# Performance work log

Measured on AMD Instinct MI355X. Metric: run time of the kernel, lower is better.

The kernel has to match this reference:

```python
import jax, jax.numpy as jnp
import numpy as np

N, TI, ENC_DIM, DEC_DIM, ATT_DIM = 32, 2000, 512, 512, 512


def setup_inputs() -> dict:
    key = jax.random.key(0)
    ks = jax.random.split(key, 8)
    enc_pad = jax.random.normal(ks[0], (N, TI, ENC_DIM), dtype=jnp.float32)
    dec_prev = jax.random.normal(ks[1], (N, DEC_DIM), dtype=jnp.float32)
    ali_prev = jax.random.uniform(ks[2], (N, TI), dtype=jnp.float32)
    # lengths in [Ti//2, Ti], force one full-length row (module uses max(enc_len) as mask width)
    enc_len = jax.random.randint(ks[3], (N,), TI // 2, TI + 1)
    enc_len = enc_len.at[0].set(TI)
    # learned params (nn.Linear layout: W [out, in])
    s_e = 1.0 / np.sqrt(ENC_DIM)
    s_d = 1.0 / np.sqrt(DEC_DIM)
    s_a = 1.0 / np.sqrt(ATT_DIM)
    W_enc = jax.random.uniform(ks[4], (ATT_DIM, ENC_DIM), minval=-s_e, maxval=s_e, dtype=jnp.float32)
    b_enc = jax.random.uniform(ks[5], (ATT_DIM,), minval=-s_e, maxval=s_e, dtype=jnp.float32)
    W_dec = jax.random.uniform(ks[6], (ATT_DIM, DEC_DIM), minval=-s_d, maxval=s_d, dtype=jnp.float32)
    w_v = jax.random.uniform(ks[7], (ATT_DIM,), minval=-s_a, maxval=s_a, dtype=jnp.float32)
    return {"enc_pad": enc_pad, "enc_len": enc_len, "dec_prev": dec_prev,
            "ali_prev": ali_prev, "W_enc": W_enc, "b_enc": b_enc,
            "W_dec": W_dec, "w_v": w_v}


def reference(enc_pad, enc_len, dec_prev, ali_prev, W_enc, b_enc, W_dec, w_v):
    # enc_part: N x Ti x A  (enc_proj with bias)
    enc_part = jnp.einsum('ntd,ad->nta', enc_pad, W_enc) + b_enc
    # dec_part: N x A  (dec_proj, no bias)
    dec_part = jnp.einsum('nd,ad->na', dec_prev, W_dec)
    # additive score e = w^T tanh(enc_part + dec_part): N x Ti
    e = jnp.einsum('nta,a->nt', jnp.tanh(enc_part + dec_part[:, None, :]), w_v)
    # padding mask: positions >= enc_len are masked
    mask = jnp.arange(e.shape[1]) >= enc_len[:, None]  # N x Ti
    e = jnp.where(mask, -jnp.inf, e)
    ali = jax.nn.softmax(e, axis=1)  # N x Ti
    ctx = jnp.einsum('nt,ntd->nd', ali, enc_pad)  # N x D_enc
    return (ali, ctx)
```

## Files before the change

### kernel.cpp

```cpp
#include <hip/hip_runtime.h>
#include <stdint.h>


#define NB  32
#define TI  2000
#define ED  512
#define AD  512
#define M_TOT (NB * TI)
#define NSPLIT 20
#define TCHUNK (TI / NSPLIT)
#define MTS 500
#define NKS 16

using f16x8 = __attribute__((ext_vector_type(8))) _Float16;
using f32x4 = __attribute__((ext_vector_type(4))) float;

#define GLD16(g, l)                                                     \
    __builtin_amdgcn_global_load_lds(                                   \
        (const __attribute__((address_space(1))) void*)(g),             \
        (__attribute__((address_space(3))) void*)(l), 16, 0, 0)

__device__ __forceinline__ float fast_tanh(float s) {
    s = fminf(fmaxf(s, -15.f), 15.f);
    float t = __expf(2.f * s);
    return __fdividef(t - 1.f, t + 1.f);
}

__device__ __forceinline__ f16x8 cvt8(float4 a, float4 b) {
    f16x8 h;
    h[0] = (_Float16)a.x; h[1] = (_Float16)a.y; h[2] = (_Float16)a.z; h[3] = (_Float16)a.w;
    h[4] = (_Float16)b.x; h[5] = (_Float16)b.y; h[6] = (_Float16)b.z; h[7] = (_Float16)b.w;
    return h;
}

__global__ void k_wconvert(const float* __restrict__ Wenc, _Float16* __restrict__ W16,
                           const float* __restrict__ dec_prev, const float* __restrict__ W_dec,
                           const float* __restrict__ b_enc, float* __restrict__ db) {
    __shared__ float xd[ED];
    int bx = blockIdx.x;
    int tid = threadIdx.x;
    if (bx >= 128) {
        int n = bx - 128;
        for (int k = tid; k < ED; k += 256) xd[k] = dec_prev[n * ED + k];
        __syncthreads();
        for (int a = tid; a < AD; a += 256) {
            const float* wr = W_dec + (size_t)a * ED;
            float s = 0.f;
#pragma unroll 8
            for (int k = 0; k < ED; k += 4) {
                float4 w = *(const float4*)(wr + k);
                s += xd[k] * w.x + xd[k + 1] * w.y + xd[k + 2] * w.z + xd[k + 3] * w.w;
            }
            db[n * AD + a] = s + b_enc[a];
        }
        return;
    }
    int idx  = bx * 4096 + tid * 16;
    int slab = idx >> 14;
    int o    = idx & 16383;
    int r    = o >> 6;
    int q    = o & 63;
    int a    = (slab >> 4) * 256 + r;
    int k    = (slab & 15) * 32 + (q >> 1);
    const float* s = Wenc + (size_t)a * ED + k;
    float4 x0 = *(const float4*)s;
    float4 x1 = *(const float4*)(s + 4);
    *(f16x8*)((char*)W16 + idx) = cvt8(x0, x1);
}

__global__ void k_decdb(const float* __restrict__ dec_prev,
                        const float* __restrict__ W_dec,
                        const float* __restrict__ b_enc,
                        float* __restrict__ db) {
    int n = blockIdx.x;
    __shared__ float xd[ED];
    for (int k = threadIdx.x; k < ED; k += 256) xd[k] = dec_prev[n * ED + k];
    __syncthreads();
    for (int a = threadIdx.x; a < AD; a += 256) {
        const float* wr = W_dec + (size_t)a * ED;
        float s = 0.f;
#pragma unroll 8
        for (int k = 0; k < ED; k += 4) {
            float4 w = *(const float4*)(wr + k);
            s += xd[k] * w.x + xd[k + 1] * w.y + xd[k + 2] * w.z + xd[k + 3] * w.w;
        }
        db[n * AD + a] = s + b_enc[a];
    }
}

__launch_bounds__(256, 2)
__global__ void k_score256(const float* __restrict__ enc, const _Float16* __restrict__ W16,
                           const float* __restrict__ db, const float* __restrict__ wv,
                           float* __restrict__ e_part) {
    __shared__ alignas(16) char As[16384];
    __shared__ alignas(16) char Bs[16384];

    int fid = blockIdx.x;
    int g = fid >> 4, r = fid & 15;
    int at2 = r >> 3;
    int mt  = g * 8 + (r & 7);
    if (mt >= MTS) return;

    const int tid  = threadIdx.x;
    const int lane = tid & 63;
    const int wn   = (tid >> 6) & 3;
    const int m0   = mt * 128;
    const int a0   = at2 * 256;
    const int lr   = lane & 15;
    const int gk   = lane >> 4;

    const char* wbase = (const char*)W16 + ((size_t)(at2 * 16) << 14);

    const int sr0 = tid >> 3;
    const int sq  = (tid & 7) * 16;

    f32x4 acc[8][4];
#pragma unroll
    for (int rb = 0; rb < 8; ++rb)
#pragma unroll
        for (int cb = 0; cb < 4; ++cb) acc[rb][cb] = (f32x4){0.f, 0.f, 0.f, 0.f};

    for (int ks = 0; ks < NKS; ++ks) {
#pragma unroll
        for (int i = 0; i < 4; ++i) {
            int rr = i * 32 + sr0;
            const float* gsrc = enc + (size_t)(m0 + rr) * ED + ks * 32
                                + ((sq ^ ((rr & 7) << 4)) >> 2);
            GLD16(gsrc, As + i * 4096 + tid * 16);
        }
        {
            const char* wsl = wbase + (ks << 14);
#pragma unroll
            for (int j = 0; j < 4; ++j)
                GLD16(wsl + j * 4096 + tid * 16, Bs + j * 4096 + tid * 16);
        }
        __syncthreads();

        {
            f16x8 aF[8], bF[4];
#pragma unroll
            for (int rb = 0; rb < 8; ++rb) {
                int row  = rb * 16 + lr;
                int base = row * 128 + gk * 32;
                int sw   = (row & 7) << 4;
                f32x4 lo = *(const f32x4*)(As + (base ^ sw));
                f32x4 hi = *(const f32x4*)(As + ((base + 16) ^ sw));
                f16x8 h;
                h[0] = (_Float16)lo[0]; h[1] = (_Float16)lo[1];
                h[2] = (_Float16)lo[2]; h[3] = (_Float16)lo[3];
                h[4] = (_Float16)hi[0]; h[5] = (_Float16)hi[1];
                h[6] = (_Float16)hi[2]; h[7] = (_Float16)hi[3];
                aF[rb] = h;
            }
#pragma unroll
            for (int cb = 0; cb < 4; ++cb) {
                int brow = wn * 64 + cb * 16 + lr;
                bF[cb] = *(const f16x8*)(Bs + brow * 64 + gk * 16);
            }
            __builtin_amdgcn_s_setprio(1);
#pragma unroll
            for (int rb = 0; rb < 8; ++rb)
#pragma unroll
                for (int cb = 0; cb < 4; ++cb)
                    acc[rb][cb] = __builtin_amdgcn_mfma_f32_16x16x32_f16(
                        aF[rb], bF[cb], acc[rb][cb], 0, 0, 0);
            __builtin_amdgcn_s_setprio(0);
        }
        __syncthreads();
    }

    float* e_red = (float*)As;
    float wvv[4];
#pragma unroll
    for (int cb = 0; cb < 4; ++cb) wvv[cb] = wv[a0 + wn * 64 + cb * 16 + lr];

#pragma unroll
    for (int rb = 0; rb < 8; ++rb) {
#pragma unroll
        for (int i = 0; i < 4; ++i) {
            int row_local = rb * 16 + gk * 4 + i;
            int m = m0 + row_local;
            int n = m / TI;
            const float* dbp = db + (size_t)n * AD + a0 + wn * 64;
            float rs = 0.f;
#pragma unroll
            for (int cb = 0; cb < 4; ++cb) {
                float s = acc[rb][cb][i] + dbp[cb * 16 + lr];
                rs += fast_tanh(s) * wvv[cb];
            }
            rs += __shfl_xor(rs, 1);
            rs += __shfl_xor(rs, 2);
            rs += __shfl_xor(rs, 4);
            rs += __shfl_xor(rs, 8);
            if (lr == 0) e_red[wn * 128 + row_local] = rs;
        }
    }
    __syncthreads();
    if (tid < 128)
        e_part[(size_t)at2 * M_TOT + m0 + tid] =
            e_red[tid] + e_red[128 + tid] + e_red[256 + tid] + e_red[384 + tid];
}

__launch_bounds__(256, 2)
__global__ void k_score_fb(const float* __restrict__ X, const float* __restrict__ W,
                           const float* __restrict__ db, const float* __restrict__ wv,
                           float* __restrict__ e_part) {
    __shared__ alignas(16) _Float16 Xs[128][72];
    __shared__ alignas(16) _Float16 Ws[128][72];
    __shared__ float e_red[2][128];

    const int tid = threadIdx.x, lane = tid & 63, wid = tid >> 6;
    const int wr = wid >> 1, wc = wid & 1;
    const int m0 = blockIdx.x * 128, a0 = blockIdx.y * 128;

    f32x4 acc[4][4];
#pragma unroll
    for (int rb = 0; rb < 4; ++rb)
#pragma unroll
        for (int cb = 0; cb < 4; ++cb) acc[rb][cb] = (f32x4){0.f, 0.f, 0.f, 0.f};

    const int lr = lane & 15;
    const int lk = (lane >> 4) << 3;

    for (int kt = 0; kt < ED; kt += 64) {
#pragma unroll
        for (int i = 0; i < 4; ++i) {
            int idx = tid + i * 256, r = idx >> 3, c = (idx & 7) << 3;
            const float* gx = X + (size_t)(m0 + r) * ED + kt + c;
            float4 x0 = *(const float4*)gx, x1 = *(const float4*)(gx + 4);
            *(f16x8*)&Xs[r][c] = cvt8(x0, x1);
            const float* gw = W + (size_t)(a0 + r) * ED + kt + c;
            float4 w0 = *(const float4*)gw, w1 = *(const float4*)(gw + 4);
            *(f16x8*)&Ws[r][c] = cvt8(w0, w1);
        }
        __syncthreads();
#pragma unroll
        for (int kb = 0; kb < 64; kb += 32) {
            f16x8 aF[4], bF[4];
#pragma unroll
            for (int rb = 0; rb < 4; ++rb) aF[rb] = *(const f16x8*)&Xs[wr * 64 + rb * 16 + lr][kb + lk];
#pragma unroll
            for (int cb = 0; cb < 4; ++cb) bF[cb] = *(const f16x8*)&Ws[wc * 64 + cb * 16 + lr][kb + lk];
#pragma unroll
            for (int rb = 0; rb < 4; ++rb)
#pragma unroll
                for (int cb = 0; cb < 4; ++cb)
                    acc[rb][cb] = __builtin_amdgcn_mfma_f32_16x16x32_f16(aF[rb], bF[cb], acc[rb][cb], 0, 0, 0);
        }
        __syncthreads();
    }

    const int lg = lane >> 4;
    float wvv[4];
#pragma unroll
    for (int cb = 0; cb < 4; ++cb) wvv[cb] = wv[a0 + wc * 64 + cb * 16 + lr];
#pragma unroll
    for (int rb = 0; rb < 4; ++rb) {
#pragma unroll
        for (int i = 0; i < 4; ++i) {
            int row_local = wr * 64 + rb * 16 + lg * 4 + i;
            int m = m0 + row_local;
            int n = m / TI;
            const float* dbp = db + (size_t)n * AD + a0 + wc * 64;
            float rs = 0.f;
#pragma unroll
            for (int cb = 0; cb < 4; ++cb) {
                float s = acc[rb][cb][i] + dbp[cb * 16 + lr];
                rs += fast_tanh(s) * wvv[cb];
            }
            rs += __shfl_xor(rs, 1);
            rs += __shfl_xor(rs, 2);
            rs += __shfl_xor(rs, 4);
            rs += __shfl_xor(rs, 8);
            if (lr == 0) e_red[wc][row_local] = rs;
        }
    }
    __syncthreads();
    if (tid < 128)
        e_part[(size_t)blockIdx.y * M_TOT + m0 + tid] = e_red[0][tid] + e_red[1][tid];
}

__global__ void k_softmax(const float* __restrict__ e_part,
                          const int* __restrict__ enc_len,
                          float* __restrict__ ali, int nparts) {
    int n = blockIdx.x;
    int len = enc_len[n];
    __shared__ float se[TI];
    __shared__ float redm[4];
    __shared__ float reds[4];
    int tid = threadIdx.x;
    int lane = tid & 63, wid = tid >> 6;

    for (int t = tid; t < TI; t += 256) {
        float s = 0.f;
        for (int p = 0; p < nparts; ++p) s += e_part[(size_t)p * M_TOT + n * TI + t];
        se[t] = s;
    }
    __syncthreads();

    float mx = -1e30f;
    for (int t = tid; t < len; t += 256) mx = fmaxf(mx, se[t]);
#pragma unroll
    for (int o = 32; o >= 1; o >>= 1) mx = fmaxf(mx, __shfl_xor(mx, o));
    if (lane == 0) redm[wid] = mx;
    __syncthreads();
    mx = fmaxf(fmaxf(redm[0], redm[1]), fmaxf(redm[2], redm[3]));

    float sm = 0.f;
    for (int t = tid; t < len; t += 256) {
        float ex = __expf(se[t] - mx);
        se[t] = ex;
        sm += ex;
    }
#pragma unroll
    for (int o = 32; o >= 1; o >>= 1) sm += __shfl_xor(sm, o);
    if (lane == 0) reds[wid] = sm;
    __syncthreads();
    float inv = 1.f / (reds[0] + reds[1] + reds[2] + reds[3]);

    for (int t = tid; t < TI; t += 256)
        ali[n * TI + t] = (t < len) ? se[t] * inv : 0.f;
}

__global__ void k_ctxpart(const float* __restrict__ enc,
                          const float* __restrict__ ali,
                          float* __restrict__ cpart) {
    int s = blockIdx.x;
    int n = blockIdx.y;
    int d0 = threadIdx.x * 2;
    const float* base = enc + ((size_t)n * TI + s * TCHUNK) * ED + d0;
    const float* ap = ali + n * TI + s * TCHUNK;
    float ax = 0.f, ay = 0.f;
#pragma unroll 4
    for (int t = 0; t < TCHUNK; ++t) {
        float a = ap[t];
        float2 v = *(const float2*)(base + (size_t)t * ED);
        ax = fmaf(a, v.x, ax);
        ay = fmaf(a, v.y, ay);
    }
    float2 r; r.x = ax; r.y = ay;
    *(float2*)&cpart[((size_t)(n * NSPLIT + s)) * ED + d0] = r;
}

__global__ void k_ctxred(const float* __restrict__ cpart, float* __restrict__ ctx) {
    int n = blockIdx.x;
    for (int d = threadIdx.x; d < ED; d += 256) {
        float sum = 0.f;
#pragma unroll
        for (int s = 0; s < NSPLIT; ++s) sum += cpart[((size_t)(n * NSPLIT + s)) * ED + d];
        ctx[(size_t)n * ED + d] = sum;
    }
}

extern "C" void kernel_launch(void* const* d_in, const int* in_sizes, int n_in,
                              void* d_out, int out_size, void* d_ws, size_t ws_size,
                              hipStream_t stream) {
    const float* enc_pad  = (const float*)d_in[0];
    const int*   enc_len  = (const int*)d_in[1];
    const float* dec_prev = (const float*)d_in[2];
    const float* W_enc    = (const float*)d_in[4];
    const float* b_enc    = (const float*)d_in[5];
    const float* W_dec    = (const float*)d_in[6];
    const float* w_v      = (const float*)d_in[7];

    float* out = (float*)d_out;
    float* ali = out;
    float* ctx = out + M_TOT;

    float* ws     = (float*)d_ws;
    float* db     = ws;
    float* e_part = ws + NB * AD;
    float* cpart  = e_part + 4 * M_TOT;
    size_t fp_floats = (size_t)NB * AD + 4 * M_TOT + (size_t)NB * NSPLIT * ED;
    _Float16* W16 = (_Float16*)((char*)d_ws + fp_floats * 4);
    size_t need = fp_floats * 4 + (size_t)512 * 1024;
    bool big = ws_size >= need;

    if (big) {
        hipLaunchKernelGGL(k_wconvert, dim3(160), dim3(256), 0, stream,
                           W_enc, W16, dec_prev, W_dec, b_enc, db);
        hipLaunchKernelGGL(k_score256, dim3(1008), dim3(256), 0, stream,
                           enc_pad, W16, db, w_v, e_part);
        hipLaunchKernelGGL(k_softmax, dim3(NB), dim3(256), 0, stream, e_part, enc_len, ali, 2);
    } else {
        hipLaunchKernelGGL(k_decdb, dim3(NB), dim3(256), 0, stream, dec_prev, W_dec, b_enc, db);
        hipLaunchKernelGGL(k_score_fb, dim3(M_TOT / 128, 4), dim3(256), 0, stream,
                           enc_pad, W_enc, db, w_v, e_part);
        hipLaunchKernelGGL(k_softmax, dim3(NB), dim3(256), 0, stream, e_part, enc_len, ali, 4);
    }
    hipLaunchKernelGGL(k_ctxpart, dim3(NSPLIT, NB), dim3(256), 0, stream, enc_pad, ali, cpart);
    hipLaunchKernelGGL(k_ctxred, dim3(NB), dim3(256), 0, stream, cpart, ctx);
}
```

Baseline: 131.9 us.

## Compute full attention width per block with double-buffered LDS staging

Each score block now covers all 512 attention columns for a 128-row tile, using 8 waves instead of two blocks per row tile. Each encoder row is therefore read from global memory once rather than twice, and the softmax pass no longer sums two partial scores. Global-to-LDS loads use two alternating buffers so the next K slice is fetched while the current one feeds the MFMAs. The pre-converted fp16 weight layout is reorganised to match. The trade-off is a much larger LDS footprint (96KB) and only 500 blocks, which may lower occupancy and leave some CUs idle in the tail.

```diff
diff --git a/kernel.cpp b/kernel.cpp
--- a/kernel.cpp
+++ b/kernel.cpp
@@ -55,13 +55,12 @@
         }
         return;
     }
-    int idx  = bx * 4096 + tid * 16;
-    int slab = idx >> 14;
-    int o    = idx & 16383;
-    int r    = o >> 6;
-    int q    = o & 63;
-    int a    = (slab >> 4) * 256 + r;
-    int k    = (slab & 15) * 32 + (q >> 1);
+    int idx = bx * 4096 + tid * 16;
+    int ks  = idx >> 15;
+    int r   = idx & 32767;
+    int gk  = r >> 13;
+    int a   = (r & 8191) >> 4;
+    int k   = ks * 32 + gk * 8;
     const float* s = Wenc + (size_t)a * ED + k;
     float4 x0 = *(const float4*)s;
     float4 x1 = *(const float4*)(s + 4);
@@ -88,103 +87,120 @@
     }
 }
 
-__launch_bounds__(256, 2)
+__launch_bounds__(512, 2)
 __global__ void k_score256(const float* __restrict__ enc, const _Float16* __restrict__ W16,
                            const float* __restrict__ db, const float* __restrict__ wv,
-                           float* __restrict__ e_part) {
-    __shared__ alignas(16) char As[16384];
-    __shared__ alignas(16) char Bs[16384];
-
-    int fid = blockIdx.x;
-    int g = fid >> 4, r = fid & 15;
-    int at2 = r >> 3;
-    int mt  = g * 8 + (r & 7);
-    if (mt >= MTS) return;
-
+                           float* __restrict__ e_out) {
+    __shared__ alignas(16) char As0[16384];
+    __shared__ alignas(16) char As1[16384];
+    __shared__ alignas(16) char Bs0[32768];
+    __shared__ alignas(16) char Bs1[32768];
+
+    const int mt   = blockIdx.x;
     const int tid  = threadIdx.x;
     const int lane = tid & 63;
-    const int wn   = (tid >> 6) & 3;
+    const int w    = tid >> 6;
+    const int wm   = w >> 2;
+    const int wn   = w & 3;
     const int m0   = mt * 128;
-    const int a0   = at2 * 256;
     const int lr   = lane & 15;
     const int gk   = lane >> 4;
 
-    const char* wbase = (const char*)W16 + ((size_t)(at2 * 16) << 14);
-
-    const int sr0 = tid >> 3;
-    const int sq  = (tid & 7) * 16;
-
-    f32x4 acc[8][4];
-#pragma unroll
-    for (int rb = 0; rb < 8; ++rb)
-#pragma unroll
-        for (int cb = 0; cb < 4; ++cb) acc[rb][cb] = (f32x4){0.f, 0.f, 0.f, 0.f};
-
-    for (int ks = 0; ks < NKS; ++ks) {
+    const int srow = tid >> 3;
+    const int sq   = (tid & 7) * 16;
+    const int sqx  = (sq ^ ((srow & 7) << 4)) >> 2;
+    const float* asrc = enc + (size_t)(m0 + srow) * ED + sqx;
+
+    const char* wbase = (const char*)W16;
+
+    f32x4 acc[4][8];
+#pragma unroll
+    for (int rb = 0; rb < 4; ++rb)
+#pragma unroll
+        for (int cb = 0; cb < 8; ++cb) acc[rb][cb] = (f32x4){0.f, 0.f, 0.f, 0.f};
+
+#define STAGE(ks, dA, dB)                                               \
+    {                                                                   \
+        GLD16(asrc + (ks) * 32,            (dA) + tid * 16);            \
+        GLD16(asrc + 64 * ED + (ks) * 32,  (dA) + 8192 + tid * 16);     \
+        const char* wsl = wbase + ((ks) << 15);                         \
+        GLD16(wsl + tid * 16,          (dB) + tid * 16);                \
+        GLD16(wsl + 8192 + tid * 16,   (dB) + 8192 + tid * 16);         \
+        GLD16(wsl + 16384 + tid * 16,  (dB) + 16384 + tid * 16);        \
+        GLD16(wsl + 24576 + tid * 16,  (dB) + 24576 + tid * 16);        \
+    }
+
+#define COMPUTE(sA, sB)                                                          \
+    {                                                                            \
+        f16x8 aF[4], bF[8];                                                      \
+        _Pragma("unroll")                                                        \
+        for (int rb = 0; rb < 4; ++rb) {                                         \
+            int row = wm * 64 + rb * 16 + lr;                                    \
+            int b0  = row * 128 + gk * 32;                                       \
+            int sw  = (row & 7) << 4;                                            \
+            f32x4 lo = *(const f32x4*)((sA) + (b0 ^ sw));                        \
+            f32x4 hi = *(const f32x4*)((sA) + ((b0 + 16) ^ sw));                 \
+            f16x8 h;                                                             \
+            h[0] = (_Float16)lo[0]; h[1] = (_Float16)lo[1];                      \
+            h[2] = (_Float16)lo[2]; h[3] = (_Float16)lo[3];                      \
+            h[4] = (_Float16)hi[0]; h[5] = (_Float16)hi[1];                      \
+            h[6] = (_Float16)hi[2]; h[7] = (_Float16)hi[3];                      \
+            aF[rb] = h;                                                          \
+        }                                                                        \
+        _Pragma("unroll")                                                        \
+        for (int cb = 0; cb < 8; ++cb) {                                         \
+            int brow = wn * 128 + cb * 16 + lr;                                  \
+            bF[cb] = *(const f16x8*)((sB) + gk * 8192 + brow * 16);              \
+        }                                                                        \
+        __builtin_amdgcn_s_setprio(1);                                           \
+        _Pragma("unroll")                                                        \
+        for (int rb = 0; rb < 4; ++rb)                                           \
+            _Pragma("unroll")                                                    \
+            for (int cb = 0; cb < 8; ++cb)                                       \
+                acc[rb][cb] = __builtin_amdgcn_mfma_f32_16x16x32_f16(            \
+                    aF[rb], bF[cb], acc[rb][cb], 0, 0, 0);                       \
+        __builtin_amdgcn_s_setprio(0);                                           \
+    }
+
+#define ITER(k, Ac, Bc, An, Bn)  STAGE(k + 1, An, Bn); COMPUTE(Ac, Bc); __syncthreads();
+
+    STAGE(0, As0, Bs0); __syncthreads();
+    ITER(0,  As0, Bs0, As1, Bs1)
+    ITER(1,  As1, Bs1, As0, Bs0)
+    ITER(2,  As0, Bs0, As1, Bs1)
+    ITER(3,  As1, Bs1, As0, Bs0)
+    ITER(4,  As0, Bs0, As1, Bs1)
+    ITER(5,  As1, Bs1, As0, Bs0)
+    ITER(6,  As0, Bs0, As1, Bs1)
+    ITER(7,  As1, Bs1, As0, Bs0)
+    ITER(8,  As0, Bs0, As1, Bs1)
+    ITER(9,  As1, Bs1, As0, Bs0)
+    ITER(10, As0, Bs0, As1, Bs1)
+    ITER(11, As1, Bs1, As0, Bs0)
+    ITER(12, As0, Bs0, As1, Bs1)
+    ITER(13, As1, Bs1, As0, Bs0)
+    ITER(14, As0, Bs0, As1, Bs1)
+    COMPUTE(As1, Bs1); __syncthreads();
+#undef ITER
+#undef COMPUTE
+#undef STAGE
+
+    float* e_red = (float*)As0;
+    float wvv[8];
+#pragma unroll
+    for (int cb = 0; cb < 8; ++cb) wvv[cb] = wv[wn * 128 + cb * 16 + lr];
+
+#pragma unroll
+    for (int rb = 0; rb < 4; ++rb) {
 #pragma unroll
         for (int i = 0; i < 4; ++i) {
-            int rr = i * 32 + sr0;
-            const float* gsrc = enc + (size_t)(m0 + rr) * ED + ks * 32
-                                + ((sq ^ ((rr & 7) << 4)) >> 2);
-            GLD16(gsrc, As + i * 4096 + tid * 16);
-        }
-        {
-            const char* wsl = wbase + (ks << 14);
-#pragma unroll
-            for (int j = 0; j < 4; ++j)
-                GLD16(wsl + j * 4096 + tid * 16, Bs + j * 4096 + tid * 16);
-        }
-        __syncthreads();
-
-        {
-            f16x8 aF[8], bF[4];
-#pragma unroll
-            for (int rb = 0; rb < 8; ++rb) {
-                int row  = rb * 16 + lr;
-                int base = row * 128 + gk * 32;
-                int sw   = (row & 7) << 4;
-                f32x4 lo = *(const f32x4*)(As + (base ^ sw));
-                f32x4 hi = *(const f32x4*)(As + ((base + 16) ^ sw));
-                f16x8 h;
-                h[0] = (_Float16)lo[0]; h[1] = (_Float16)lo[1];
-                h[2] = (_Float16)lo[2]; h[3] = (_Float16)lo[3];
-                h[4] = (_Float16)hi[0]; h[5] = (_Float16)hi[1];
-                h[6] = (_Float16)hi[2]; h[7] = (_Float16)hi[3];
-                aF[rb] = h;
-            }
-#pragma unroll
-            for (int cb = 0; cb < 4; ++cb) {
-                int brow = wn * 64 + cb * 16 + lr;
-                bF[cb] = *(const f16x8*)(Bs + brow * 64 + gk * 16);
-            }
-            __builtin_amdgcn_s_setprio(1);
-#pragma unroll
-            for (int rb = 0; rb < 8; ++rb)
-#pragma unroll
-                for (int cb = 0; cb < 4; ++cb)
-                    acc[rb][cb] = __builtin_amdgcn_mfma_f32_16x16x32_f16(
-                        aF[rb], bF[cb], acc[rb][cb], 0, 0, 0);
-            __builtin_amdgcn_s_setprio(0);
-        }
-        __syncthreads();
-    }
-
-    float* e_red = (float*)As;
-    float wvv[4];
-#pragma unroll
-    for (int cb = 0; cb < 4; ++cb) wvv[cb] = wv[a0 + wn * 64 + cb * 16 + lr];
-
-#pragma unroll
-    for (int rb = 0; rb < 8; ++rb) {
-#pragma unroll
-        for (int i = 0; i < 4; ++i) {
-            int row_local = rb * 16 + gk * 4 + i;
+            int row_local = wm * 64 + rb * 16 + gk * 4 + i;
             int m = m0 + row_local;
             int n = m / TI;
-            const float* dbp = db + (size_t)n * AD + a0 + wn * 64;
+            const float* dbp = db + (size_t)n * AD + wn * 128;
             float rs = 0.f;
 #pragma unroll
-            for (int cb = 0; cb < 4; ++cb) {
+            for (int cb = 0; cb < 8; ++cb) {
                 float s = acc[rb][cb][i] + dbp[cb * 16 + lr];
                 rs += fast_tanh(s) * wvv[cb];
             }
@@ -197,7 +213,7 @@
     }
     __syncthreads();
     if (tid < 128)
-        e_part[(size_t)at2 * M_TOT + m0 + tid] =
+        e_out[m0 + tid] =
             e_red[tid] + e_red[128 + tid] + e_red[256 + tid] + e_red[384 + tid];
 }
 
@@ -379,9 +395,9 @@
     if (big) {
         hipLaunchKernelGGL(k_wconvert, dim3(160), dim3(256), 0, stream,
                            W_enc, W16, dec_prev, W_dec, b_enc, db);
-        hipLaunchKernelGGL(k_score256, dim3(1008), dim3(256), 0, stream,
+        hipLaunchKernelGGL(k_score256, dim3(MTS), dim3(512), 0, stream,
                            enc_pad, W16, db, w_v, e_part);
-        hipLaunchKernelGGL(k_softmax, dim3(NB), dim3(256), 0, stream, e_part, enc_len, ali, 2);
+        hipLaunchKernelGGL(k_softmax, dim3(NB), dim3(256), 0, stream, e_part, enc_len, ali, 1);
     } else {
         hipLaunchKernelGGL(k_decdb, dim3(NB), dim3(256), 0, stream, dec_prev, W_dec, b_enc, db);
         hipLaunchKernelGGL(k_score_fb, dim3(M_TOT / 128, 4), dim3(256), 0, stream,
```

After: 119.9 us. 9.1% less time.
